# Performance work log

Hardware: AMD Instinct MI355X
Metric: run time of the kernel (lower is better)

## Reference

```python
import jax, jax.numpy as jnp
import numpy as np

DIM = 1024
HEADS = 16
DIM_HEAD = 64
INNER = HEADS * DIM_HEAD  # 1024
SCALE = DIM_HEAD ** (-0.5)
EPS = 1e-5


def _layernorm(x, g, b):
    mu = jnp.mean(x, axis=-1, keepdims=True)
    var = jnp.mean(jnp.square(x - mu), axis=-1, keepdims=True)
    return (x - mu) * jax.lax.rsqrt(var + EPS) * g + b


def _split_heads(t):
    # b t n (h d) -> b h t n d
    b, T, n, _ = t.shape
    return t.reshape(b, T, n, HEADS, DIM_HEAD).transpose(0, 3, 1, 2, 4)


def setup_inputs() -> dict:
    key = jax.random.key(0)
    ks = jax.random.split(key, 9)
    b, T, n1, n2 = 8, 4, 1024, 64
    x = jax.random.normal(ks[0], (b, T, n1, DIM), dtype=jnp.float32)
    latents = jax.random.normal(ks[1], (b, T, n2, DIM), dtype=jnp.float32)
    g_media = 1.0 + 0.02 * jax.random.normal(ks[2], (DIM,), dtype=jnp.float32)
    b_media = 0.02 * jax.random.normal(ks[3], (DIM,), dtype=jnp.float32)
    g_lat = 1.0 + 0.02 * jax.random.normal(ks[4], (DIM,), dtype=jnp.float32)
    b_lat = 0.02 * jax.random.normal(ks[5], (DIM,), dtype=jnp.float32)
    s = DIM ** (-0.5)
    Wq = jax.random.normal(ks[6], (DIM, INNER), dtype=jnp.float32) * s
    Wkv = jax.random.normal(ks[7], (DIM, 2 * INNER), dtype=jnp.float32) * s
    Wo = jax.random.normal(ks[8], (INNER, DIM), dtype=jnp.float32) * (INNER ** (-0.5))
    return {"x": x, "latents": latents, "g_media": g_media, "b_media": b_media,
            "g_lat": g_lat, "b_lat": b_lat, "Wq": Wq, "Wkv": Wkv, "Wo": Wo}


def reference(x, latents, g_media, b_media, g_lat, b_lat, Wq, Wkv, Wo):
    x = _layernorm(x, g_media, b_media)          # (b, T, n1, D)
    lat = _layernorm(latents, g_lat, b_lat)      # (b, T, n2, D)

    q = lat @ Wq                                 # (b, T, n2, inner)
    kv_input = jnp.concatenate((x, lat), axis=-2)  # (b, T, n1+n2, D)
    kv = kv_input @ Wkv                          # (b, T, n1+n2, 2*inner)
    k, v = jnp.split(kv, 2, axis=-1)

    q = _split_heads(q) * SCALE                  # (b, h, T, n2, d)
    k = _split_heads(k)                          # (b, h, T, n1+n2, d)
    v = _split_heads(v)

    sim = jnp.einsum('bhtid,bhtjd->bhtij', q, k)  # (b, h, T, n2, n1+n2)
    attn = jax.nn.softmax(sim, axis=-1)           # stable (amax subtracted)
    out = jnp.einsum('bhtij,bhtjd->bhtid', attn, v)

    # b h t n d -> b t n (h d)
    b, h, T, n, d = out.shape
    out = out.transpose(0, 2, 3, 1, 4).reshape(b, T, n, h * d)
    return out @ Wo
```

## Files before the change

kernel.cpp:

```cpp
#include <hip/hip_runtime.h>

#define DEVI __device__ __forceinline__

typedef unsigned short u16;
typedef unsigned int u32;

using bf16x8 = __attribute__((ext_vector_type(8))) short;
using f32x4  = __attribute__((ext_vector_type(4))) float;

DEVI u16 f2bf(float f) {
  u32 u = __builtin_bit_cast(u32, f);
  u32 r = (u + 0x7fffu + ((u >> 16) & 1u)) >> 16;
  return (u16)r;
}

DEVI void gl_lds16(const u16* g, u16* l) {
  __builtin_amdgcn_global_load_lds(
      (const __attribute__((address_space(1))) u32*)g,
      (__attribute__((address_space(3))) u32*)l, 16, 0, 0);
}

__global__ __launch_bounds__(256) void ln_kernel(
    const float* __restrict__ x, const float* __restrict__ lat,
    const float* __restrict__ gm, const float* __restrict__ bm,
    const float* __restrict__ gl, const float* __restrict__ bl,
    u16* __restrict__ kvin, u16* __restrict__ latb)
{
  int row = blockIdx.x;
  int bt = row / 1088, r = row % 1088;
  const float *src, *g, *b;
  bool is_lat = (r >= 1024);
  if (!is_lat) { src = x + ((size_t)bt*1024 + r)*1024; g = gm; b = bm; }
  else         { src = lat + ((size_t)bt*64 + (r-1024))*1024; g = gl; b = bl; }
  int tid = threadIdx.x;
  float4 v = *(const float4*)(src + tid*4);
  float s1 = v.x+v.y+v.z+v.w;
  float s2 = v.x*v.x+v.y*v.y+v.z*v.z+v.w*v.w;
  for (int off=32; off; off>>=1){ s1 += __shfl_down(s1,off); s2 += __shfl_down(s2,off); }
  __shared__ float red[2][4];
  int w = tid>>6, lane = tid&63;
  if (lane==0){ red[0][w]=s1; red[1][w]=s2; }
  __syncthreads();
  s1 = red[0][0]+red[0][1]+red[0][2]+red[0][3];
  s2 = red[1][0]+red[1][1]+red[1][2]+red[1][3];
  float mu = s1 * (1.f/1024.f);
  float var = s2 * (1.f/1024.f) - mu*mu;
  float rstd = rsqrtf(var + 1e-5f);
  float4 gv = *(const float4*)(g + tid*4);
  float4 bv = *(const float4*)(b + tid*4);
  ushort4 o;
  o.x = f2bf((v.x-mu)*rstd*gv.x + bv.x);
  o.y = f2bf((v.y-mu)*rstd*gv.y + bv.y);
  o.z = f2bf((v.z-mu)*rstd*gv.z + bv.z);
  o.w = f2bf((v.w-mu)*rstd*gv.w + bv.w);
  *(ushort4*)(kvin + (size_t)row*1024 + tid*4) = o;
  if (is_lat) *(ushort4*)(latb + ((size_t)(bt*64 + (r-1024)))*1024 + tid*4) = o;
}

__global__ __launch_bounds__(256) void transpose_cast(
    const float* __restrict__ in, u16* __restrict__ out, int R, int C)
{
  __shared__ float t[32][33];
  int bx = blockIdx.x*32, by = blockIdx.y*32;
  int tx = threadIdx.x & 31, ty = threadIdx.x >> 5;
  for (int k=0;k<32;k+=8) t[ty+k][tx] = in[(size_t)(by+ty+k)*C + bx+tx];
  __syncthreads();
  for (int k=0;k<32;k+=8) out[(size_t)(bx+ty+k)*R + by+tx] = f2bf(t[tx][ty+k]);
}

__global__ __launch_bounds__(256,2) void gemm_bt_f32(
    const u16* __restrict__ A, const u16* __restrict__ BT,
    float* __restrict__ C, int N, int K)
{
  __shared__ u16 lA[128*32];
  __shared__ u16 lB[128*32];
  int tid = threadIdx.x;
  int w = tid>>6, lane = tid&63;
  int li = lane&15, lg = lane>>4;
  int m0 = blockIdx.y*128, n0 = blockIdx.x*128;
  int wr = (w>>1)*64, wc = (w&1)*64;
  f32x4 acc[4][4] = {};
  int sr = lane>>2;
  int sk = ((lane&3) ^ ((lane>>3)&3))*8;
  const int rchunk = (lg ^ ((li>>1)&3))*8;
  const u16* pa = A  + (size_t)(m0 + w*32 + sr)*K + sk;
  const u16* pb = BT + (size_t)(n0 + w*32 + sr)*K + sk;
  u16* la0 = lA + (w*2)*512; u16* la1 = lA + (w*2+1)*512;
  u16* lb0 = lB + (w*2)*512; u16* lb1 = lB + (w*2+1)*512;
  for (int k0=0; k0<K; k0+=32) {
    gl_lds16(pa,        la0);
    gl_lds16(pa + 16*(size_t)K, la1);
    gl_lds16(pb,        lb0);
    gl_lds16(pb + 16*(size_t)K, lb1);
    pa += 32; pb += 32;
    __syncthreads();
    bf16x8 af[4], bfr[4];
    #pragma unroll
    for (int m=0;m<4;++m) af[m]  = *(const bf16x8*)(lA + (wr + m*16 + li)*32 + rchunk);
    #pragma unroll
    for (int n=0;n<4;++n) bfr[n] = *(const bf16x8*)(lB + (wc + n*16 + li)*32 + rchunk);
    #pragma unroll
    for (int m=0;m<4;++m)
      #pragma unroll
      for (int n=0;n<4;++n)
        acc[m][n] = __builtin_amdgcn_mfma_f32_16x16x32_bf16(af[m], bfr[n], acc[m][n], 0,0,0);
    __syncthreads();
  }
  #pragma unroll
  for (int m=0;m<4;++m)
    #pragma unroll
    for (int n=0;n<4;++n) {
      int row = m0 + wr + m*16 + lg*4;
      int col = n0 + wc + n*16 + li;
      #pragma unroll
      for (int rg=0;rg<4;++rg)
        C[(size_t)(row+rg)*N + col] = acc[m][n][rg];
    }
}

__global__ __launch_bounds__(512,2) void gemm256_kvq(
    const u16* __restrict__ A, const u16* __restrict__ BT,
    const u16* __restrict__ Aq, const u16* __restrict__ BTq,
    u16* __restrict__ kb, u16* __restrict__ vt, u16* __restrict__ qb)
{
  __shared__ u16 lds[2][2][2][256][32];
  const int tid = threadIdx.x;
  const int w = tid>>6, lane = tid&63;
  const int li = lane&15, lg = lane>>4;
  const int wm = w>>2, wn = w&3;
  const int bid = blockIdx.x;
  const int swz = (bid&7)*140 + (bid>>3);
  const bool is_q = (swz >= 1088);
  const u16* Asrc; const u16* Bsrc; int m0, n0;
  if (!is_q) { Asrc = A;  Bsrc = BT;  m0 = (swz>>3)*256;        n0 = (swz&7)*256; }
  else       { int qt = swz-1088; Asrc = Aq; Bsrc = BTq; m0 = (qt>>2)*256; n0 = (qt&3)*256; }
  const int srow = lane>>2;
  const int scol = ((lane&3) ^ ((lane>>3)&3))*8;
  const int rchunk = (lg ^ ((li>>1)&3))*8;

#define STAGE(b, mat, kh, kt) do {                                            \
    const u16* _s = (mat) ? Bsrc : Asrc;                                      \
    const int _base = (mat) ? n0 : m0;                                        \
    _Pragma("unroll")                                                         \
    for (int L=0; L<2; ++L) {                                                 \
      const int _r = L*128 + w*16;                                            \
      gl_lds16(_s + (size_t)(_base + _r + srow)*1024 + (kt)*64 + (kh)*32 + scol, \
               &lds[b][mat][kh][_r][0]);                                      \
    }                                                                         \
  } while(0)
#define BARRIER() asm volatile("s_barrier" ::: "memory")
#define LGKM0()   do { asm volatile("s_waitcnt lgkmcnt(0)" ::: "memory"); \
                       __builtin_amdgcn_sched_barrier(0); } while(0)
#define VM4()     asm volatile("s_waitcnt vmcnt(4)" ::: "memory")

  f32x4 acc[8][4] = {};

  STAGE(0,0,0,0); STAGE(0,1,0,0); STAGE(0,0,1,0); STAGE(0,1,1,0);
  VM4(); BARRIER();

  for (int j=0; j<16; ++j) {
    const int c = j&1;
    const int kt = (j<15) ? j+1 : 15;
    bf16x8 a[4], b0[4], b1[4];

    #pragma unroll
    for (int mf=0; mf<4; ++mf)
      a[mf] = *(const bf16x8*)&lds[c][0][0][wm*128 + mf*16 + li][rchunk];
    #pragma unroll
    for (int nf=0; nf<4; ++nf)
      b0[nf] = *(const bf16x8*)&lds[c][1][0][wn*64 + nf*16 + li][rchunk];
    STAGE(c^1,0,0,kt);
    BARRIER(); LGKM0();
    __builtin_amdgcn_s_setprio(1);
    #pragma unroll
    for (int mf=0; mf<4; ++mf)
      #pragma unroll
      for (int nf=0; nf<4; ++nf)
        acc[mf][nf] = __builtin_amdgcn_mfma_f32_16x16x32_bf16(a[mf], b0[nf], acc[mf][nf], 0,0,0);
    __builtin_amdgcn_s_setprio(0);
    BARRIER();

    #pragma unroll
    for (int mf=0; mf<4; ++mf)
      a[mf] = *(const bf16x8*)&lds[c][0][0][wm*128 + 64 + mf*16 + li][rchunk];
    STAGE(c^1,1,0,kt);
    VM4();
    BARRIER(); LGKM0();
    __builtin_amdgcn_s_setprio(1);
    #pragma unroll
    for (int mf=0; mf<4; ++mf)
      #pragma unroll
      for (int nf=0; nf<4; ++nf)
        acc[4+mf][nf] = __builtin_amdgcn_mfma_f32_16x16x32_bf16(a[mf], b0[nf], acc[4+mf][nf], 0,0,0);
    __builtin_amdgcn_s_setprio(0);
    BARRIER();

    #pragma unroll
    for (int mf=0; mf<4; ++mf)
      a[mf] = *(const bf16x8*)&lds[c][0][1][wm*128 + mf*16 + li][rchunk];
    #pragma unroll
    for (int nf=0; nf<4; ++nf)
      b1[nf] = *(const bf16x8*)&lds[c][1][1][wn*64 + nf*16 + li][rchunk];
    STAGE(c^1,0,1,kt);
    BARRIER(); LGKM0();
    __builtin_amdgcn_s_setprio(1);
    #pragma unroll
    for (int mf=0; mf<4; ++mf)
      #pragma unroll
      for (int nf=0; nf<4; ++nf)
        acc[mf][nf] = __builtin_amdgcn_mfma_f32_16x16x32_bf16(a[mf], b1[nf], acc[mf][nf], 0,0,0);
    __builtin_amdgcn_s_setprio(0);
    BARRIER();

    #pragma unroll
    for (int mf=0; mf<4; ++mf)
      a[mf] = *(const bf16x8*)&lds[c][0][1][wm*128 + 64 + mf*16 + li][rchunk];
    STAGE(c^1,1,1,kt);
    VM4();
    BARRIER(); LGKM0();
    __builtin_amdgcn_s_setprio(1);
    #pragma unroll
    for (int mf=0; mf<4; ++mf)
      #pragma unroll
      for (int nf=0; nf<4; ++nf)
        acc[4+mf][nf] = __builtin_amdgcn_mfma_f32_16x16x32_bf16(a[mf], b1[nf], acc[4+mf][nf], 0,0,0);
    __builtin_amdgcn_s_setprio(0);
    BARRIER();
  }
#undef STAGE
#undef BARRIER
#undef LGKM0
#undef VM4

  if (is_q) {
    #pragma unroll
    for (int am=0; am<8; ++am)
      #pragma unroll
      for (int nf=0; nf<4; ++nf) {
        int row = m0 + wm*128 + am*16 + lg*4;
        int col = n0 + wn*64 + nf*16 + li;
        #pragma unroll
        for (int rg=0; rg<4; ++rg)
          qb[(size_t)(row+rg)*1024 + col] = f2bf(acc[am][nf][rg]*0.125f);
      }
  } else if (n0 < 1024) {
    #pragma unroll
    for (int am=0; am<8; ++am)
      #pragma unroll
      for (int nf=0; nf<4; ++nf) {
        int row = m0 + wm*128 + am*16 + lg*4;
        int col = n0 + wn*64 + nf*16 + li;
        #pragma unroll
        for (int rg=0; rg<4; ++rg)
          kb[(size_t)(row+rg)*1024 + col] = f2bf(acc[am][nf][rg]);
      }
  } else {
    #pragma unroll
    for (int am=0; am<8; ++am)
      #pragma unroll
      for (int nf=0; nf<4; ++nf) {
        int r0 = m0 + wm*128 + am*16 + lg*4;
        int cc = n0 + wn*64 + nf*16 + li - 1024;
        int bt = r0/1088, jj = r0 - bt*1088;
        ushort4 o;
        o.x = f2bf(acc[am][nf][0]); o.y = f2bf(acc[am][nf][1]);
        o.z = f2bf(acc[am][nf][2]); o.w = f2bf(acc[am][nf][3]);
        *(ushort4*)(vt + ((size_t)(bt*1024 + cc))*1088 + jj) = o;
      }
  }
}

__global__ __launch_bounds__(256,2) void attn_kernel(
    const u16* __restrict__ qbuf, const u16* __restrict__ kbuf,
    const u16* __restrict__ vT, u16* __restrict__ aout)
{
  __shared__ u16 p_im[4][16][72];
  int blk = blockIdx.x;
  int bt = blk >> 4, h = blk & 15;
  int w = threadIdx.x>>6, lane = threadIdx.x&63;
  int li = lane&15, lg = lane>>4;
  const u16* qrow = qbuf + ((size_t)(bt*64 + w*16 + li))*1024 + h*64;
  bf16x8 qf0 = *(const bf16x8*)(qrow + lg*8);
  bf16x8 qf1 = *(const bf16x8*)(qrow + 32 + lg*8);
  float mrun = -INFINITY, lrun = 0.f;
  f32x4 oacc[4] = {};
  const u16* kbase = kbuf + (size_t)bt*1088*1024 + h*64;
  const u16* vbase = vT + ((size_t)(bt*1024 + h*64))*1088;
  for (int c=0; c<17; ++c) {
    int j0 = c*64;
    f32x4 s[4] = {};
    #pragma unroll
    for (int jt=0; jt<4; ++jt) {
      const u16* krow = kbase + (size_t)(j0 + jt*16 + li)*1024;
      bf16x8 k0 = *(const bf16x8*)(krow + lg*8);
      bf16x8 k1 = *(const bf16x8*)(krow + 32 + lg*8);
      s[jt] = __builtin_amdgcn_mfma_f32_16x16x32_bf16(k0, qf0, s[jt], 0,0,0);
      s[jt] = __builtin_amdgcn_mfma_f32_16x16x32_bf16(k1, qf1, s[jt], 0,0,0);
    }
    float cm = -INFINITY;
    #pragma unroll
    for (int jt=0;jt<4;++jt)
      cm = fmaxf(cm, fmaxf(fmaxf(s[jt][0], s[jt][1]), fmaxf(s[jt][2], s[jt][3])));
    cm = fmaxf(cm, __shfl_xor(cm,16));
    cm = fmaxf(cm, __shfl_xor(cm,32));
    float mnew = fmaxf(mrun, cm);
    float sf = __expf(mrun - mnew);
    float ls = 0.f;
    #pragma unroll
    for (int jt=0;jt<4;++jt) {
      float p0 = __expf(s[jt][0]-mnew), p1 = __expf(s[jt][1]-mnew);
      float p2 = __expf(s[jt][2]-mnew), p3 = __expf(s[jt][3]-mnew);
      ls += p0+p1+p2+p3;
      ushort4 pk; pk.x = f2bf(p0); pk.y = f2bf(p1); pk.z = f2bf(p2); pk.w = f2bf(p3);
      *(ushort4*)&p_im[w][li][jt*16 + lg*4] = pk;
    }
    ls += __shfl_xor(ls,16);
    ls += __shfl_xor(ls,32);
    lrun = lrun*sf + ls;
    mrun = mnew;
    float sfr[4];
    #pragma unroll
    for (int rg=0;rg<4;++rg) sfr[rg] = __shfl(sf, lg*4+rg);
    #pragma unroll
    for (int dt=0;dt<4;++dt) {
      oacc[dt][0]*=sfr[0]; oacc[dt][1]*=sfr[1]; oacc[dt][2]*=sfr[2]; oacc[dt][3]*=sfr[3];
    }
    bf16x8 pa0 = *(const bf16x8*)&p_im[w][li][lg*8];
    bf16x8 pa1 = *(const bf16x8*)&p_im[w][li][32 + lg*8];
    #pragma unroll
    for (int dt=0;dt<4;++dt) {
      const u16* vrow = vbase + (size_t)(dt*16 + li)*1088 + j0;
      bf16x8 v0 = *(const bf16x8*)(vrow + lg*8);
      bf16x8 v1 = *(const bf16x8*)(vrow + 32 + lg*8);
      oacc[dt] = __builtin_amdgcn_mfma_f32_16x16x32_bf16(pa0, v0, oacc[dt], 0,0,0);
      oacc[dt] = __builtin_amdgcn_mfma_f32_16x16x32_bf16(pa1, v1, oacc[dt], 0,0,0);
    }
  }
  float linv[4];
  #pragma unroll
  for (int rg=0;rg<4;++rg) linv[rg] = 1.f / __shfl(lrun, lg*4+rg);
  u16* orow = aout + ((size_t)(bt*64 + w*16))*1024 + h*64;
  #pragma unroll
  for (int dt=0;dt<4;++dt)
    #pragma unroll
    for (int rg=0;rg<4;++rg)
      orow[(size_t)(lg*4+rg)*1024 + dt*16 + li] = f2bf(oacc[dt][rg]*linv[rg]);
}

extern "C" void kernel_launch(void* const* d_in, const int* in_sizes, int n_in,
                              void* d_out, int out_size, void* d_ws, size_t ws_size,
                              hipStream_t stream) {
  const float* x   = (const float*)d_in[0];
  const float* lat = (const float*)d_in[1];
  const float* gm  = (const float*)d_in[2];
  const float* bm  = (const float*)d_in[3];
  const float* gl  = (const float*)d_in[4];
  const float* bl  = (const float*)d_in[5];
  const float* Wq  = (const float*)d_in[6];
  const float* Wkv = (const float*)d_in[7];
  const float* Wo  = (const float*)d_in[8];
  float* out = (float*)d_out;

  char* ws = (char*)d_ws;
  const size_t KV_BYTES = (size_t)32*1088*1024*2;
  u16* kvin = (u16*)(ws);
  u16* kbuf = (u16*)(ws + KV_BYTES);
  u16* vT   = (u16*)(ws + 2*KV_BYTES);
  u16* latb = (u16*)(ws + 3*KV_BYTES);
  u16* qbuf = (u16*)(ws + 3*KV_BYTES + (size_t)4194304);
  u16* aout = (u16*)(ws + 3*KV_BYTES + (size_t)2*4194304);
  u16* wqT  = (u16*)(ws + 3*KV_BYTES + (size_t)3*4194304);
  u16* wkvT = (u16*)(ws + 3*KV_BYTES + (size_t)3*4194304 + 2097152);
  u16* woT  = (u16*)(ws + 3*KV_BYTES + (size_t)3*4194304 + 2097152 + 4194304);

  ln_kernel<<<dim3(32*1088), dim3(256), 0, stream>>>(x, lat, gm, bm, gl, bl, kvin, latb);
  transpose_cast<<<dim3(32,32), dim3(256), 0, stream>>>(Wq,  wqT,  1024, 1024);
  transpose_cast<<<dim3(64,32), dim3(256), 0, stream>>>(Wkv, wkvT, 1024, 2048);
  transpose_cast<<<dim3(32,32), dim3(256), 0, stream>>>(Wo,  woT,  1024, 1024);

  gemm256_kvq<<<dim3(1120), dim3(512), 0, stream>>>(kvin, wkvT, latb, wqT, kbuf, vT, qbuf);
  attn_kernel<<<dim3(512), dim3(256), 0, stream>>>(qbuf, kbuf, vT, aout);
  gemm_bt_f32<<<dim3(8,16), dim3(256), 0, stream>>>(aout, woT, out, 1024, 1024);
}
```

Baseline: 303.6 us.

## Double-buffer K/V tiles in LDS for attention, merge weight transposes, retile output GEMM

The attention kernel now copies each 64-key chunk of K and V^T into a double-buffered LDS tile with async global-to-LDS loads, prefetching the next chunk while the current one is computed. Before, every wave read K and V directly from global memory. The three weight transpose launches are merged into one launch. The output GEMM uses 128x64 tiles, which gives 256 blocks instead of 128 so more CUs are busy. The cost is more LDS per attention block and an extra barrier on every chunk.

```diff
diff --git a/kernel.cpp b/kernel.cpp
--- a/kernel.cpp
+++ b/kernel.cpp
@@ -57,65 +57,23 @@
   if (is_lat) *(ushort4*)(latb + ((size_t)(bt*64 + (r-1024)))*1024 + tid*4) = o;
 }
 
-__global__ __launch_bounds__(256) void transpose_cast(
-    const float* __restrict__ in, u16* __restrict__ out, int R, int C)
+__global__ __launch_bounds__(256) void transpose_all(
+    const float* __restrict__ Wq, const float* __restrict__ Wkv,
+    const float* __restrict__ Wo,
+    u16* __restrict__ wqT, u16* __restrict__ wkvT, u16* __restrict__ woT)
 {
   __shared__ float t[32][33];
-  int bx = blockIdx.x*32, by = blockIdx.y*32;
+  int bxg = blockIdx.x;
+  const float* in; u16* outp; int C, bxi;
+  if (bxg < 32)      { in = Wq;  outp = wqT;  C = 1024; bxi = bxg; }
+  else if (bxg < 96) { in = Wkv; outp = wkvT; C = 2048; bxi = bxg - 32; }
+  else               { in = Wo;  outp = woT;  C = 1024; bxi = bxg - 96; }
+  const int R = 1024;
+  int bx = bxi*32, by = blockIdx.y*32;
   int tx = threadIdx.x & 31, ty = threadIdx.x >> 5;
   for (int k=0;k<32;k+=8) t[ty+k][tx] = in[(size_t)(by+ty+k)*C + bx+tx];
   __syncthreads();
-  for (int k=0;k<32;k+=8) out[(size_t)(bx+ty+k)*R + by+tx] = f2bf(t[tx][ty+k]);
-}
-
-__global__ __launch_bounds__(256,2) void gemm_bt_f32(
-    const u16* __restrict__ A, const u16* __restrict__ BT,
-    float* __restrict__ C, int N, int K)
-{
-  __shared__ u16 lA[128*32];
-  __shared__ u16 lB[128*32];
-  int tid = threadIdx.x;
-  int w = tid>>6, lane = tid&63;
-  int li = lane&15, lg = lane>>4;
-  int m0 = blockIdx.y*128, n0 = blockIdx.x*128;
-  int wr = (w>>1)*64, wc = (w&1)*64;
-  f32x4 acc[4][4] = {};
-  int sr = lane>>2;
-  int sk = ((lane&3) ^ ((lane>>3)&3))*8;
-  const int rchunk = (lg ^ ((li>>1)&3))*8;
-  const u16* pa = A  + (size_t)(m0 + w*32 + sr)*K + sk;
-  const u16* pb = BT + (size_t)(n0 + w*32 + sr)*K + sk;
-  u16* la0 = lA + (w*2)*512; u16* la1 = lA + (w*2+1)*512;
-  u16* lb0 = lB + (w*2)*512; u16* lb1 = lB + (w*2+1)*512;
-  for (int k0=0; k0<K; k0+=32) {
-    gl_lds16(pa,        la0);
-    gl_lds16(pa + 16*(size_t)K, la1);
-    gl_lds16(pb,        lb0);
-    gl_lds16(pb + 16*(size_t)K, lb1);
-    pa += 32; pb += 32;
-    __syncthreads();
-    bf16x8 af[4], bfr[4];
-    #pragma unroll
-    for (int m=0;m<4;++m) af[m]  = *(const bf16x8*)(lA + (wr + m*16 + li)*32 + rchunk);
-    #pragma unroll
-    for (int n=0;n<4;++n) bfr[n] = *(const bf16x8*)(lB + (wc + n*16 + li)*32 + rchunk);
-    #pragma unroll
-    for (int m=0;m<4;++m)
-      #pragma unroll
-      for (int n=0;n<4;++n)
-        acc[m][n] = __builtin_amdgcn_mfma_f32_16x16x32_bf16(af[m], bfr[n], acc[m][n], 0,0,0);
-    __syncthreads();
-  }
-  #pragma unroll
-  for (int m=0;m<4;++m)
-    #pragma unroll
-    for (int n=0;n<4;++n) {
-      int row = m0 + wr + m*16 + lg*4;
-      int col = n0 + wc + n*16 + li;
-      #pragma unroll
-      for (int rg=0;rg<4;++rg)
-        C[(size_t)(row+rg)*N + col] = acc[m][n][rg];
-    }
+  for (int k=0;k<32;k+=8) outp[(size_t)(bx+ty+k)*R + by+tx] = f2bf(t[tx][ty+k]);
 }
 
 __global__ __launch_bounds__(512,2) void gemm256_kvq(
@@ -270,10 +228,61 @@
   }
 }
 
+__global__ __launch_bounds__(256,4) void gemm_out(
+    const u16* __restrict__ A, const u16* __restrict__ BT,
+    float* __restrict__ C)
+{
+  __shared__ u16 lA[128*32];
+  __shared__ u16 lB[64*32];
+  const int tid = threadIdx.x;
+  const int w = tid>>6, lane = tid&63;
+  const int li = lane&15, lg = lane>>4;
+  const int wm = w>>1, wn = w&1;
+  int m0 = blockIdx.y*128, n0 = blockIdx.x*64;
+  const int srow = tid>>2;
+  const int scol = ((tid&3) ^ ((tid>>3)&3))*8;
+  const int rchunk = (lg ^ ((li>>1)&3))*8;
+  u16* dA0 = lA + (w*16)*32;
+  u16* dA1 = lA + (64 + w*16)*32;
+  u16* dB  = lB + (w*16)*32;
+  const u16* pa0 = A  + (size_t)(m0 + srow)*1024 + scol;
+  const u16* pa1 = A  + (size_t)(m0 + 64 + srow)*1024 + scol;
+  const u16* pb  = BT + (size_t)(n0 + srow)*1024 + scol;
+  f32x4 acc[4][2] = {};
+  for (int k=0; k<32; ++k) {
+    gl_lds16(pa0 + k*32, dA0);
+    gl_lds16(pa1 + k*32, dA1);
+    if (srow < 64) gl_lds16(pb + k*32, dB);
+    __syncthreads();
+    bf16x8 af[4], bf[2];
+    #pragma unroll
+    for (int m=0;m<4;++m) af[m] = *(const bf16x8*)(lA + (wm*64 + m*16 + li)*32 + rchunk);
+    #pragma unroll
+    for (int n=0;n<2;++n) bf[n] = *(const bf16x8*)(lB + (wn*32 + n*16 + li)*32 + rchunk);
+    #pragma unroll
+    for (int m=0;m<4;++m)
+      #pragma unroll
+      for (int n=0;n<2;++n)
+        acc[m][n] = __builtin_amdgcn_mfma_f32_16x16x32_bf16(af[m], bf[n], acc[m][n], 0,0,0);
+    __syncthreads();
+  }
+  #pragma unroll
+  for (int m=0;m<4;++m)
+    #pragma unroll
+    for (int n=0;n<2;++n) {
+      int row = m0 + wm*64 + m*16 + lg*4;
+      int col = n0 + wn*32 + n*16 + li;
+      #pragma unroll
+      for (int rg=0;rg<4;++rg)
+        C[(size_t)(row+rg)*1024 + col] = acc[m][n][rg];
+    }
+}
+
 __global__ __launch_bounds__(256,2) void attn_kernel(
     const u16* __restrict__ qbuf, const u16* __restrict__ kbuf,
     const u16* __restrict__ vT, u16* __restrict__ aout)
 {
+  __shared__ u16 kv_lds[2][2][64][64];
   __shared__ u16 p_im[4][16][72];
   int blk = blockIdx.x;
   int bt = blk >> 4, h = blk & 15;
@@ -282,18 +291,39 @@
   const u16* qrow = qbuf + ((size_t)(bt*64 + w*16 + li))*1024 + h*64;
   bf16x8 qf0 = *(const bf16x8*)(qrow + lg*8);
   bf16x8 qf1 = *(const bf16x8*)(qrow + 32 + lg*8);
+  const int srl = lane>>3;
+  const int sch = (lane&7) ^ srl;
+  const u16* kgbase = kbuf + ((size_t)(bt*1088) + w*16 + srl)*1024 + h*64 + sch*8;
+  const u16* vgbase = vT + ((size_t)(bt*1024 + h*64 + w*16 + srl))*1088 + sch*8;
+  const int rc0 = ((lg     ^ (li&7)))*8;
+  const int rc1 = (((4+lg) ^ (li&7)))*8;
+
+#define STAGE_KV(b, c) do {                                                    \
+    int _j0 = (c)*64;                                                          \
+    _Pragma("unroll")                                                          \
+    for (int i=0;i<2;++i) {                                                    \
+      gl_lds16(kgbase + (size_t)(_j0 + i*8)*1024, &kv_lds[b][0][w*16+i*8][0]); \
+      gl_lds16(vgbase + _j0 + (size_t)(i*8)*1088, &kv_lds[b][1][w*16+i*8][0]); \
+    }                                                                          \
+  } while(0)
+
   float mrun = -INFINITY, lrun = 0.f;
   f32x4 oacc[4] = {};
-  const u16* kbase = kbuf + (size_t)bt*1088*1024 + h*64;
-  const u16* vbase = vT + ((size_t)(bt*1024 + h*64))*1088;
+
+  STAGE_KV(0,0);
+  __syncthreads();
+
   for (int c=0; c<17; ++c) {
-    int j0 = c*64;
+    int cb = c&1;
+    if (c<16) STAGE_KV(cb^1, c+1);
+    const u16* kl = &kv_lds[cb][0][0][0];
+    const u16* vl = &kv_lds[cb][1][0][0];
     f32x4 s[4] = {};
     #pragma unroll
     for (int jt=0; jt<4; ++jt) {
-      const u16* krow = kbase + (size_t)(j0 + jt*16 + li)*1024;
-      bf16x8 k0 = *(const bf16x8*)(krow + lg*8);
-      bf16x8 k1 = *(const bf16x8*)(krow + 32 + lg*8);
+      const u16* kr = kl + (jt*16+li)*64;
+      bf16x8 k0 = *(const bf16x8*)(kr + rc0);
+      bf16x8 k1 = *(const bf16x8*)(kr + rc1);
       s[jt] = __builtin_amdgcn_mfma_f32_16x16x32_bf16(k0, qf0, s[jt], 0,0,0);
       s[jt] = __builtin_amdgcn_mfma_f32_16x16x32_bf16(k1, qf1, s[jt], 0,0,0);
     }
@@ -329,13 +359,16 @@
     bf16x8 pa1 = *(const bf16x8*)&p_im[w][li][32 + lg*8];
     #pragma unroll
     for (int dt=0;dt<4;++dt) {
-      const u16* vrow = vbase + (size_t)(dt*16 + li)*1088 + j0;
-      bf16x8 v0 = *(const bf16x8*)(vrow + lg*8);
-      bf16x8 v1 = *(const bf16x8*)(vrow + 32 + lg*8);
+      const u16* vr = vl + (dt*16+li)*64;
+      bf16x8 v0 = *(const bf16x8*)(vr + rc0);
+      bf16x8 v1 = *(const bf16x8*)(vr + rc1);
       oacc[dt] = __builtin_amdgcn_mfma_f32_16x16x32_bf16(pa0, v0, oacc[dt], 0,0,0);
       oacc[dt] = __builtin_amdgcn_mfma_f32_16x16x32_bf16(pa1, v1, oacc[dt], 0,0,0);
     }
+    __syncthreads();
   }
+#undef STAGE_KV
+
   float linv[4];
   #pragma unroll
   for (int rg=0;rg<4;++rg) linv[rg] = 1.f / __shfl(lrun, lg*4+rg);
@@ -374,11 +407,9 @@
   u16* woT  = (u16*)(ws + 3*KV_BYTES + (size_t)3*4194304 + 2097152 + 4194304);
 
   ln_kernel<<<dim3(32*1088), dim3(256), 0, stream>>>(x, lat, gm, bm, gl, bl, kvin, latb);
-  transpose_cast<<<dim3(32,32), dim3(256), 0, stream>>>(Wq,  wqT,  1024, 1024);
-  transpose_cast<<<dim3(64,32), dim3(256), 0, stream>>>(Wkv, wkvT, 1024, 2048);
-  transpose_cast<<<dim3(32,32), dim3(256), 0, stream>>>(Wo,  woT,  1024, 1024);
+  transpose_all<<<dim3(128,32), dim3(256), 0, stream>>>(Wq, Wkv, Wo, wqT, wkvT, woT);
 
   gemm256_kvq<<<dim3(1120), dim3(512), 0, stream>>>(kvin, wkvT, latb, wqT, kbuf, vT, qbuf);
   attn_kernel<<<dim3(512), dim3(256), 0, stream>>>(qbuf, kbuf, vT, aout);
-  gemm_bt_f32<<<dim3(8,16), dim3(256), 0, stream>>>(aout, woT, out, 1024, 1024);
-}
+  gemm_out<<<dim3(16,16), dim3(256), 0, stream>>>(aout, woT, out);
+}
```

After: 262.6 us. 13.5% less time.
